# Optimization experiments

Hardware: AMD Instinct MI355X
Metric: run time of the kernel (lower is better)

## Reference

```python
import jax, jax.numpy as jnp
import numpy as np

HEADS = 20  # head_dim = 1280 // 20 = 64
LORA_SCALE = 1.0


def setup_inputs() -> dict:
    key = jax.random.key(0)
    ks = jax.random.split(key, 16)
    B, S, C, R = 2, 2048, 1280, 4
    w = 0.02  # keep activations numerically tame
    inp = {
        "x": jax.random.normal(ks[0], (B, S, C), jnp.float32),
        "Wq": jax.random.normal(ks[1], (C, C), jnp.float32) * w,
        "Wk": jax.random.normal(ks[2], (C, C), jnp.float32) * w,
        "Wv": jax.random.normal(ks[3], (C, C), jnp.float32) * w,
        "Wo": jax.random.normal(ks[4], (C, C), jnp.float32) * w,
        "bo": jnp.zeros((C,), jnp.float32),
        "Aq": jax.random.normal(ks[5], (R, C), jnp.float32) * w,
        "Bq": jax.random.normal(ks[6], (C, R), jnp.float32) * w,
        "Ak": jax.random.normal(ks[7], (R, C), jnp.float32) * w,
        "Bk": jax.random.normal(ks[8], (C, R), jnp.float32) * w,
        "Av": jax.random.normal(ks[9], (R, C), jnp.float32) * w,
        "Bv": jax.random.normal(ks[10], (C, R), jnp.float32) * w,
        "Ao": jax.random.normal(ks[11], (R, C), jnp.float32) * w,
        "Bo": jax.random.normal(ks[12], (C, R), jnp.float32) * w,
    }
    return inp


def _lora(x, A, B):
    # LoRALinearLayer: up(down(x)); network_alpha=None -> no extra scaling
    return (x @ A.T) @ B.T


def reference(x, Wq, Wk, Wv, Wo, bo, Aq, Bq, Ak, Bk, Av, Bv, Ao, Bo):
    B, S, C = x.shape
    H = HEADS
    D = C // H
    # base projections + LoRA updates (self-attention: encoder_hidden_states = x)
    q = x @ Wq.T + LORA_SCALE * _lora(x, Aq, Bq)
    k = x @ Wk.T + LORA_SCALE * _lora(x, Ak, Bk)
    v = x @ Wv.T + LORA_SCALE * _lora(x, Av, Bv)
    # head split: [B, S, H, D]
    q = q.reshape(B, S, H, D)
    k = k.reshape(B, S, H, D)
    v = v.reshape(B, S, H, D)
    # explicit scores + softmax (attn.get_attention_scores), scale = 1/sqrt(D)
    scale = 1.0 / jnp.sqrt(jnp.asarray(D, x.dtype))
    scores = jnp.einsum("bshd,bthd->bhst", q, k) * scale  # [B, H, S, S]
    probs = jax.nn.softmax(scores, axis=-1)
    ctx = jnp.einsum("bhst,bthd->bshd", probs, v).reshape(B, S, C)
    # output projection (+bias) + LoRA; dropout is identity at eval
    out = ctx @ Wo.T + bo + LORA_SCALE * _lora(ctx, Ao, Bo)
    return out
```

## Files before the change

### kernel.cpp

```cpp
#include <hip/hip_runtime.h>

#define BATCH 2
#define SEQ   2048
#define CH    1280
#define NH    20
#define HD    64
#define BS    (BATCH*SEQ)
#define RK    4

typedef __attribute__((ext_vector_type(2)))  float floatx2;
typedef __attribute__((ext_vector_type(4)))  short bf16x4;
typedef __attribute__((ext_vector_type(8)))  short bf16x8;
typedef __attribute__((ext_vector_type(16))) float floatx16;

__device__ __forceinline__ floatx16 mfma32(bf16x8 a, bf16x8 b, floatx16 c) {
    return __builtin_amdgcn_mfma_f32_32x32x16_bf16(a, b, c, 0, 0, 0);
}
__device__ __forceinline__ floatx16 mfma32k8(bf16x4 a, bf16x4 b, floatx16 c) {
    return __builtin_amdgcn_mfma_f32_32x32x8bf16_1k(a, b, c, 0, 0, 0);
}

__device__ __forceinline__ unsigned short f2bf(float f) {
    unsigned int u = __float_as_uint(f);
    u += 0x7fffu + ((u >> 16) & 1u);
    return (unsigned short)(u >> 16);
}
__device__ __forceinline__ unsigned int packbf(float hi, float lo) {
    unsigned int a = __float_as_uint(hi) + 0x8000u;
    unsigned int b = __float_as_uint(lo) + 0x8000u;
    return __builtin_amdgcn_perm(a, b, 0x07060302u);
}
__device__ __forceinline__ float fexp2(float x) {
#if __has_builtin(__builtin_amdgcn_exp2f)
    return __builtin_amdgcn_exp2f(x);
#else
    return exp2f(x);
#endif
}

__device__ __forceinline__ void cp16(const unsigned short* g, unsigned short* l) {
    __builtin_amdgcn_global_load_lds(
        (const __attribute__((address_space(1))) unsigned int*)g,
        (__attribute__((address_space(3))) unsigned int*)l, 16, 0, 0);
}

__global__ __launch_bounds__(256) void fold_weights(
    const float* __restrict__ Wq, const float* __restrict__ Wk,
    const float* __restrict__ Wv, const float* __restrict__ Wo,
    const float* __restrict__ Aq, const float* __restrict__ Bq,
    const float* __restrict__ Ak, const float* __restrict__ Bk,
    const float* __restrict__ Av, const float* __restrict__ Bv,
    const float* __restrict__ Ao, const float* __restrict__ Bo,
    unsigned short* __restrict__ wq_bf, unsigned short* __restrict__ wk_bf,
    unsigned short* __restrict__ wv_bf, unsigned short* __restrict__ wo_bf)
{
    int e = blockIdx.x * 256 + threadIdx.x;
    int which = blockIdx.y;
    int i = e / CH, j = e % CH;
    const float *W, *A, *Bm;
    unsigned short* o;
    if (which == 0)      { W = Wq; A = Aq; Bm = Bq; o = wq_bf; }
    else if (which == 1) { W = Wk; A = Ak; Bm = Bk; o = wk_bf; }
    else if (which == 2) { W = Wv; A = Av; Bm = Bv; o = wv_bf; }
    else                 { W = Wo; A = Ao; Bm = Bo; o = wo_bf; }
    float acc = W[e];
#pragma unroll
    for (int r = 0; r < RK; r++) acc += Bm[i * RK + r] * A[r * CH + j];
    o[e] = f2bf(acc);
}

__global__ __launch_bounds__(256) void cast_x(const float* __restrict__ x,
                                              unsigned short* __restrict__ xb)
{
    int idx = (blockIdx.x * 256 + threadIdx.x) * 4;
    float4 v = *(const float4*)(x + idx);
    ushort4 o;
    o.x = f2bf(v.x); o.y = f2bf(v.y); o.z = f2bf(v.z); o.w = f2bf(v.w);
    *(ushort4*)(xb + idx) = o;
}

template<bool OUTF>
__device__ __forceinline__ void gemm128(
    const unsigned short* __restrict__ A, const unsigned short* __restrict__ B,
    unsigned short* __restrict__ obf, float* __restrict__ of,
    const float* __restrict__ bias, float oscale)
{
    __shared__ __align__(16) unsigned short sa[128 * 64];
    __shared__ __align__(16) unsigned short sb[128 * 64];
    const int tid = threadIdx.x;
    const int wav = tid >> 6, lane = tid & 63;
    const int n32 = lane & 31, half = lane >> 5;
    const int wr = wav >> 1, wc = wav & 1;
    const int M0 = blockIdx.y * 128, N0 = blockIdx.x * 128;

    const unsigned short* ga[4]; const unsigned short* gb[4];
    unsigned short* la[4]; unsigned short* lb[4];
#pragma unroll
    for (int g = 0; g < 4; g++) {
        int s = g * 256 + tid;
        int row = s >> 3, cc = (s & 7) ^ (row & 7);
        ga[g] = A + (size_t)(M0 + row) * CH + cc * 8;
        gb[g] = B + (size_t)(N0 + row) * CH + cc * 8;
        la[g] = sa + (size_t)(g * 256 + wav * 64) * 8;
        lb[g] = sb + (size_t)(g * 256 + wav * 64) * 8;
    }

    const int arow0 = wr * 64 + n32, brow0 = wc * 64 + n32;

    floatx16 acc[2][2];
#pragma unroll
    for (int mt = 0; mt < 2; mt++)
#pragma unroll
        for (int nt = 0; nt < 2; nt++)
#pragma unroll
            for (int r = 0; r < 16; r++) acc[mt][nt][r] = 0.f;

    for (int k0 = 0; k0 < CH; k0 += 64) {
#pragma unroll
        for (int g = 0; g < 4; g++) { cp16(ga[g], la[g]); cp16(gb[g], lb[g]); }
#pragma unroll
        for (int g = 0; g < 4; g++) { ga[g] += 64; gb[g] += 64; }
        __syncthreads();

        bf16x8 av[2][4], bv[2][4];
#pragma unroll
        for (int mt = 0; mt < 2; mt++) {
            const int ar = arow0 + mt * 32, br = brow0 + mt * 32;
#pragma unroll
            for (int ks = 0; ks < 4; ks++) {
                const int cc = ks * 2 + half;
                av[mt][ks] = *(const bf16x8*)(sa + ar * 64 + ((cc ^ (ar & 7)) << 3));
                bv[mt][ks] = *(const bf16x8*)(sb + br * 64 + ((cc ^ (br & 7)) << 3));
            }
        }
#pragma unroll
        for (int ks = 0; ks < 4; ks++)
#pragma unroll
            for (int mt = 0; mt < 2; mt++)
#pragma unroll
                for (int nt = 0; nt < 2; nt++)
                    acc[mt][nt] = mfma32(av[mt][ks], bv[nt][ks], acc[mt][nt]);
        __syncthreads();
    }

#pragma unroll
    for (int mt = 0; mt < 2; mt++) {
#pragma unroll
        for (int nt = 0; nt < 2; nt++) {
            const int col = N0 + wc * 64 + nt * 32 + n32;
            const float bv2 = OUTF ? bias[col] : 0.f;
#pragma unroll
            for (int r = 0; r < 16; r++) {
                size_t row = (size_t)(M0 + wr * 64 + mt * 32 +
                                      (r & 3) + 8 * (r >> 2) + 4 * half);
                if (OUTF) of[row * CH + col] = acc[mt][nt][r] + bv2;
                else      obf[row * CH + col] = f2bf(acc[mt][nt][r] * oscale);
            }
        }
    }
}

__global__ __launch_bounds__(256) void gemm_qkv(
    const unsigned short* __restrict__ xb,
    const unsigned short* __restrict__ wq, const unsigned short* __restrict__ wk,
    const unsigned short* __restrict__ wv,
    unsigned short* __restrict__ q, unsigned short* __restrict__ k,
    unsigned short* __restrict__ v)
{
    const unsigned short* w = blockIdx.z == 0 ? wq : blockIdx.z == 1 ? wk : wv;
    unsigned short* o = blockIdx.z == 0 ? q : blockIdx.z == 1 ? k : v;
    float scale = blockIdx.z == 0 ? 0.18033688011112042f : 1.0f;
    gemm128<false>(xb, w, o, nullptr, nullptr, scale);
}

__global__ __launch_bounds__(256) void gemm_o(
    const unsigned short* __restrict__ c_bf, const unsigned short* __restrict__ wo,
    const float* __restrict__ bias, float* __restrict__ out)
{
    gemm128<true>(c_bf, wo, nullptr, out, bias, 1.0f);
}

__global__ __launch_bounds__(256) void transpose_v(
    const unsigned short* __restrict__ v, unsigned short* __restrict__ vt)
{
    __shared__ unsigned short lds[32][34];
    const int s0 = blockIdx.x * 32;
    const int d0 = blockIdx.y * 32;
    const int bh = blockIdx.z, b = bh / NH, h = bh % NH;
    const int c = threadIdx.x & 31;
    const int rbase = threadIdx.x >> 5;
#pragma unroll
    for (int i = 0; i < 4; i++) {
        int r = rbase + i * 8;
        lds[r][c] = v[(size_t)(b * SEQ + s0 + r) * CH + h * HD + d0 + c];
    }
    __syncthreads();
    const int cperm = (c & ~12) | ((c & 4) << 1) | ((c & 8) >> 1);
#pragma unroll
    for (int i = 0; i < 4; i++) {
        int r = rbase + i * 8;
        vt[(size_t)(bh * HD + d0 + r) * SEQ + s0 + cperm] = lds[c][r];
    }
}

__global__ __launch_bounds__(256) void attention(
    const unsigned short* __restrict__ q, const unsigned short* __restrict__ k,
    const unsigned short* __restrict__ vt, unsigned short* __restrict__ c_bf)
{
    __shared__ __align__(16) unsigned short k_lds[128 * 64];
    __shared__ __align__(16) unsigned short v_lds[64 * 128];

    const int tid = threadIdx.x, wav = tid >> 6, lane = tid & 63;
    const int n32 = lane & 31, half = lane >> 5;
    const int q0 = blockIdx.x * 128;
    const int bh = blockIdx.y, b = bh / NH, h = bh % NH;

    const size_t qrow = (size_t)(b * SEQ + q0 + wav * 32 + n32);
    bf16x8 qf[4];
#pragma unroll
    for (int f = 0; f < 4; f++)
        qf[f] = *(const bf16x8*)(q + qrow * CH + h * HD + f * 16 + half * 8);

    const unsigned short* gk[4]; const unsigned short* gv[4];
    unsigned short* lk[4]; unsigned short* lv[4];
#pragma unroll
    for (int g = 0; g < 4; g++) {
        int s = g * 256 + tid;
        int rowk = s >> 3, cck = (s & 7) ^ (rowk & 7);
        gk[g] = k + (size_t)(b * SEQ + rowk) * CH + h * HD + cck * 8;
        lk[g] = k_lds + (size_t)(g * 256 + wav * 64) * 8;
        int rowv = s >> 4, ccv = (s & 15) ^ (rowv & 15);
        gv[g] = vt + (size_t)(bh * HD + rowv) * SEQ + ccv * 8;
        lv[g] = v_lds + (size_t)(g * 256 + wav * 64) * 8;
    }

    floatx2 ps = {0.f, 0.f};
    floatx16 acc[2];
#pragma unroll
    for (int dt = 0; dt < 2; dt++)
#pragma unroll
        for (int r = 0; r < 16; r++) acc[dt][r] = 0.f;

    for (int t0 = 0; t0 < SEQ; t0 += 128) {
#pragma unroll
        for (int g = 0; g < 4; g++) { cp16(gk[g], lk[g]); cp16(gv[g], lv[g]); }
#pragma unroll
        for (int g = 0; g < 4; g++) { gk[g] += (size_t)128 * CH; gv[g] += 128; }
        __syncthreads();

#pragma unroll
        for (int kt = 0; kt < 4; kt++) {
            const int keyrow = kt * 32 + n32;
            const unsigned short* kr = k_lds + keyrow * 64;
            floatx16 st;
#pragma unroll
            for (int r = 0; r < 16; r++) st[r] = 0.f;
#pragma unroll
            for (int f = 0; f < 4; f++) {
                int phys = (2 * f + half) ^ (keyrow & 7);
                bf16x8 kf = *(const bf16x8*)(kr + phys * 8);
                st = mfma32(kf, qf[f], st);
            }

            float p[16];
#pragma unroll
            for (int r = 0; r < 16; r++) p[r] = fexp2(st[r]);
            unsigned int pk[8];
#pragma unroll
            for (int j = 0; j < 8; j++) {
                ps += (floatx2){p[2 * j], p[2 * j + 1]};
                pk[j] = packbf(p[2 * j + 1], p[2 * j]);
            }

#pragma unroll
            for (int dt = 0; dt < 2; dt++) {
                const int drow = dt * 32 + n32;
                const unsigned short* vr = v_lds + drow * 128;
#pragma unroll
                for (int pp = 0; pp < 2; pp++) {
                    int ct = kt * 4 + pp * 2 + half;
                    int phys = ct ^ (drow & 15);
                    union { bf16x8 v8; bf16x4 v4[2]; } vv;
                    vv.v8 = *(const bf16x8*)(vr + phys * 8);
                    union { unsigned int u[2]; bf16x4 v; } pb0, pb1;
                    pb0.u[0] = pk[4 * pp + 0]; pb0.u[1] = pk[4 * pp + 1];
                    pb1.u[0] = pk[4 * pp + 2]; pb1.u[1] = pk[4 * pp + 3];
                    acc[dt] = mfma32k8(vv.v4[0], pb0.v, acc[dt]);
                    acc[dt] = mfma32k8(vv.v4[1], pb1.v, acc[dt]);
                }
            }
        }
        __syncthreads();
    }

    float psum = ps.x + ps.y;
    float tot = psum + __shfl_xor(psum, 32, 64);
    float rinv = __frcp_rn(tot);
    const size_t obase = qrow * CH + h * HD;
#pragma unroll
    for (int dt = 0; dt < 2; dt++) {
#pragma unroll
        for (int jj = 0; jj < 4; jj++) {
            int d = dt * 32 + 8 * jj + 4 * half;
            uint2 o2;
            o2.x = packbf(acc[dt][4 * jj + 1] * rinv, acc[dt][4 * jj + 0] * rinv);
            o2.y = packbf(acc[dt][4 * jj + 3] * rinv, acc[dt][4 * jj + 2] * rinv);
            *(uint2*)(c_bf + obase + d) = o2;
        }
    }
}

extern "C" void kernel_launch(void* const* d_in, const int* in_sizes, int n_in,
                              void* d_out, int out_size, void* d_ws, size_t ws_size,
                              hipStream_t stream)
{
    const float* x  = (const float*)d_in[0];
    const float* Wq = (const float*)d_in[1];
    const float* Wk = (const float*)d_in[2];
    const float* Wv = (const float*)d_in[3];
    const float* Wo = (const float*)d_in[4];
    const float* bo = (const float*)d_in[5];
    const float* Aq = (const float*)d_in[6];
    const float* Bq = (const float*)d_in[7];
    const float* Ak = (const float*)d_in[8];
    const float* Bk = (const float*)d_in[9];
    const float* Av = (const float*)d_in[10];
    const float* Bv = (const float*)d_in[11];
    const float* Ao = (const float*)d_in[12];
    const float* Bo = (const float*)d_in[13];
    float* out = (float*)d_out;

    char* ws = (char*)d_ws;
    size_t off = 0;
    auto alloc = [&](size_t bytes) -> void* {
        void* p = ws + off; off += (bytes + 255) & ~(size_t)255; return p;
    };
    const size_t WB = (size_t)CH * CH, XB = (size_t)BS * CH;
    unsigned short* wq_bf = (unsigned short*)alloc(WB * 2);
    unsigned short* wk_bf = (unsigned short*)alloc(WB * 2);
    unsigned short* wv_bf = (unsigned short*)alloc(WB * 2);
    unsigned short* wo_bf = (unsigned short*)alloc(WB * 2);
    unsigned short* x_bf  = (unsigned short*)alloc(XB * 2);
    unsigned short* q_bf  = (unsigned short*)alloc(XB * 2);
    unsigned short* k_bf  = (unsigned short*)alloc(XB * 2);
    unsigned short* v_bf  = (unsigned short*)alloc(XB * 2);
    unsigned short* vt_bf = (unsigned short*)alloc(XB * 2);
    unsigned short* c_bf  = (unsigned short*)alloc(XB * 2);
    (void)ws_size; (void)n_in; (void)in_sizes; (void)out_size;

    fold_weights<<<dim3(CH * CH / 256, 4), 256, 0, stream>>>(
        Wq, Wk, Wv, Wo, Aq, Bq, Ak, Bk, Av, Bv, Ao, Bo,
        wq_bf, wk_bf, wv_bf, wo_bf);

    cast_x<<<dim3(BS * CH / 1024), 256, 0, stream>>>(x, x_bf);

    gemm_qkv<<<dim3(CH / 128, BS / 128, 3), 256, 0, stream>>>(
        x_bf, wq_bf, wk_bf, wv_bf, q_bf, k_bf, v_bf);

    transpose_v<<<dim3(SEQ / 32, 2, BATCH * NH), 256, 0, stream>>>(v_bf, vt_bf);

    attention<<<dim3(SEQ / 128, BATCH * NH), 256, 0, stream>>>(
        q_bf, k_bf, vt_bf, c_bf);

    gemm_o<<<dim3(CH / 128, BS / 128), 256, 0, stream>>>(c_bf, wo_bf, bo, out);
}
```

Before: 289.7 us.

## Merge prep kernels and cut attention register pressure for higher occupancy

Merges the weight-folding and x-cast kernels into one launch, which removes a kernel launch and its tail. In the attention kernel it replaces the per-group pointer arrays with a single base pointer plus constant offsets. It also computes exp and packing per half-tile right before use rather than materialising all 16 probabilities at once. It sets launch_bounds to 4 blocks per CU, so register usage is capped to raise occupancy, at some risk of spills.

```diff
diff --git a/kernel.cpp b/kernel.cpp
--- a/kernel.cpp
+++ b/kernel.cpp
@@ -44,7 +44,11 @@
         (__attribute__((address_space(3))) unsigned int*)l, 16, 0, 0);
 }
 
-__global__ __launch_bounds__(256) void fold_weights(
+#define FOLD_BLOCKS (CH * CH / 256)
+#define CAST_BLOCKS (BS * CH / 1024)
+
+__global__ __launch_bounds__(256) void prep(
+    const float* __restrict__ x,
     const float* __restrict__ Wq, const float* __restrict__ Wk,
     const float* __restrict__ Wv, const float* __restrict__ Wo,
     const float* __restrict__ Aq, const float* __restrict__ Bq,
@@ -52,31 +56,31 @@
     const float* __restrict__ Av, const float* __restrict__ Bv,
     const float* __restrict__ Ao, const float* __restrict__ Bo,
     unsigned short* __restrict__ wq_bf, unsigned short* __restrict__ wk_bf,
-    unsigned short* __restrict__ wv_bf, unsigned short* __restrict__ wo_bf)
-{
-    int e = blockIdx.x * 256 + threadIdx.x;
-    int which = blockIdx.y;
-    int i = e / CH, j = e % CH;
-    const float *W, *A, *Bm;
-    unsigned short* o;
-    if (which == 0)      { W = Wq; A = Aq; Bm = Bq; o = wq_bf; }
-    else if (which == 1) { W = Wk; A = Ak; Bm = Bk; o = wk_bf; }
-    else if (which == 2) { W = Wv; A = Av; Bm = Bv; o = wv_bf; }
-    else                 { W = Wo; A = Ao; Bm = Bo; o = wo_bf; }
-    float acc = W[e];
-#pragma unroll
-    for (int r = 0; r < RK; r++) acc += Bm[i * RK + r] * A[r * CH + j];
-    o[e] = f2bf(acc);
-}
-
-__global__ __launch_bounds__(256) void cast_x(const float* __restrict__ x,
-                                              unsigned short* __restrict__ xb)
-{
-    int idx = (blockIdx.x * 256 + threadIdx.x) * 4;
-    float4 v = *(const float4*)(x + idx);
-    ushort4 o;
-    o.x = f2bf(v.x); o.y = f2bf(v.y); o.z = f2bf(v.z); o.w = f2bf(v.w);
-    *(ushort4*)(xb + idx) = o;
+    unsigned short* __restrict__ wv_bf, unsigned short* __restrict__ wo_bf,
+    unsigned short* __restrict__ xb)
+{
+    const int bx = blockIdx.x;
+    if (bx < 4 * FOLD_BLOCKS) {
+        int which = bx / FOLD_BLOCKS;
+        int e = (bx % FOLD_BLOCKS) * 256 + threadIdx.x;
+        int i = e / CH, j = e % CH;
+        const float *W, *A, *Bm;
+        unsigned short* o;
+        if (which == 0)      { W = Wq; A = Aq; Bm = Bq; o = wq_bf; }
+        else if (which == 1) { W = Wk; A = Ak; Bm = Bk; o = wk_bf; }
+        else if (which == 2) { W = Wv; A = Av; Bm = Bv; o = wv_bf; }
+        else                 { W = Wo; A = Ao; Bm = Bo; o = wo_bf; }
+        float acc = W[e];
+#pragma unroll
+        for (int r = 0; r < RK; r++) acc += Bm[i * RK + r] * A[r * CH + j];
+        o[e] = f2bf(acc);
+    } else {
+        int idx = ((bx - 4 * FOLD_BLOCKS) * 256 + threadIdx.x) * 4;
+        float4 v = *(const float4*)(x + idx);
+        ushort4 o;
+        o.x = f2bf(v.x); o.y = f2bf(v.y); o.z = f2bf(v.z); o.w = f2bf(v.w);
+        *(ushort4*)(xb + idx) = o;
+    }
 }
 
 template<bool OUTF>
@@ -203,7 +207,7 @@
     }
 }
 
-__global__ __launch_bounds__(256) void attention(
+__global__ __launch_bounds__(256, 4) void attention(
     const unsigned short* __restrict__ q, const unsigned short* __restrict__ k,
     const unsigned short* __restrict__ vt, unsigned short* __restrict__ c_bf)
 {
@@ -221,18 +225,12 @@
     for (int f = 0; f < 4; f++)
         qf[f] = *(const bf16x8*)(q + qrow * CH + h * HD + f * 16 + half * 8);
 
-    const unsigned short* gk[4]; const unsigned short* gv[4];
-    unsigned short* lk[4]; unsigned short* lv[4];
-#pragma unroll
-    for (int g = 0; g < 4; g++) {
-        int s = g * 256 + tid;
-        int rowk = s >> 3, cck = (s & 7) ^ (rowk & 7);
-        gk[g] = k + (size_t)(b * SEQ + rowk) * CH + h * HD + cck * 8;
-        lk[g] = k_lds + (size_t)(g * 256 + wav * 64) * 8;
-        int rowv = s >> 4, ccv = (s & 15) ^ (rowv & 15);
-        gv[g] = vt + (size_t)(bh * HD + rowv) * SEQ + ccv * 8;
-        lv[g] = v_lds + (size_t)(g * 256 + wav * 64) * 8;
-    }
+    const int rowk = tid >> 3, cck = (tid & 7) ^ (rowk & 7);
+    const int rowv = tid >> 4, ccv = (tid & 15) ^ (rowv & 15);
+    const unsigned short* gk0 = k + (size_t)(b * SEQ + rowk) * CH + h * HD + cck * 8;
+    const unsigned short* gv0 = vt + (size_t)(bh * HD + rowv) * SEQ + ccv * 8;
+    unsigned short* lk0 = k_lds + (size_t)(wav * 64) * 8;
+    unsigned short* lv0 = v_lds + (size_t)(wav * 64) * 8;
 
     floatx2 ps = {0.f, 0.f};
     floatx16 acc[2];
@@ -243,9 +241,11 @@
 
     for (int t0 = 0; t0 < SEQ; t0 += 128) {
 #pragma unroll
-        for (int g = 0; g < 4; g++) { cp16(gk[g], lk[g]); cp16(gv[g], lv[g]); }
-#pragma unroll
-        for (int g = 0; g < 4; g++) { gk[g] += (size_t)128 * CH; gv[g] += 128; }
+        for (int g = 0; g < 4; g++) {
+            cp16(gk0 + (size_t)g * 32 * CH, lk0 + g * 2048);
+            cp16(gv0 + g * 16 * SEQ, lv0 + g * 2048);
+        }
+        gk0 += (size_t)128 * CH; gv0 += 128;
         __syncthreads();
 
 #pragma unroll
@@ -262,29 +262,27 @@
                 st = mfma32(kf, qf[f], st);
             }
 
-            float p[16];
-#pragma unroll
-            for (int r = 0; r < 16; r++) p[r] = fexp2(st[r]);
-            unsigned int pk[8];
-#pragma unroll
-            for (int j = 0; j < 8; j++) {
-                ps += (floatx2){p[2 * j], p[2 * j + 1]};
-                pk[j] = packbf(p[2 * j + 1], p[2 * j]);
-            }
-
-#pragma unroll
-            for (int dt = 0; dt < 2; dt++) {
-                const int drow = dt * 32 + n32;
-                const unsigned short* vr = v_lds + drow * 128;
-#pragma unroll
-                for (int pp = 0; pp < 2; pp++) {
+#pragma unroll
+            for (int pp = 0; pp < 2; pp++) {
+                float p[8];
+#pragma unroll
+                for (int r = 0; r < 8; r++) p[r] = fexp2(st[8 * pp + r]);
+                unsigned int pk[4];
+#pragma unroll
+                for (int j = 0; j < 4; j++) {
+                    ps += (floatx2){p[2 * j], p[2 * j + 1]};
+                    pk[j] = packbf(p[2 * j + 1], p[2 * j]);
+                }
+                union { unsigned int u[2]; bf16x4 v; } pb0, pb1;
+                pb0.u[0] = pk[0]; pb0.u[1] = pk[1];
+                pb1.u[0] = pk[2]; pb1.u[1] = pk[3];
+#pragma unroll
+                for (int dt = 0; dt < 2; dt++) {
+                    const int drow = dt * 32 + n32;
                     int ct = kt * 4 + pp * 2 + half;
                     int phys = ct ^ (drow & 15);
                     union { bf16x8 v8; bf16x4 v4[2]; } vv;
-                    vv.v8 = *(const bf16x8*)(vr + phys * 8);
-                    union { unsigned int u[2]; bf16x4 v; } pb0, pb1;
-                    pb0.u[0] = pk[4 * pp + 0]; pb0.u[1] = pk[4 * pp + 1];
-                    pb1.u[0] = pk[4 * pp + 2]; pb1.u[1] = pk[4 * pp + 3];
+                    vv.v8 = *(const bf16x8*)(v_lds + drow * 128 + phys * 8);
                     acc[dt] = mfma32k8(vv.v4[0], pb0.v, acc[dt]);
                     acc[dt] = mfma32k8(vv.v4[1], pb1.v, acc[dt]);
                 }
@@ -348,11 +346,9 @@
     unsigned short* c_bf  = (unsigned short*)alloc(XB * 2);
     (void)ws_size; (void)n_in; (void)in_sizes; (void)out_size;
 
-    fold_weights<<<dim3(CH * CH / 256, 4), 256, 0, stream>>>(
-        Wq, Wk, Wv, Wo, Aq, Bq, Ak, Bk, Av, Bv, Ao, Bo,
-        wq_bf, wk_bf, wv_bf, wo_bf);
-
-    cast_x<<<dim3(BS * CH / 1024), 256, 0, stream>>>(x, x_bf);
+    prep<<<dim3(4 * FOLD_BLOCKS + CAST_BLOCKS), 256, 0, stream>>>(
+        x, Wq, Wk, Wv, Wo, Aq, Bq, Ak, Bk, Av, Bv, Ao, Bo,
+        wq_bf, wk_bf, wv_bf, wo_bf, x_bf);
 
     gemm_qkv<<<dim3(CH / 128, BS / 128, 3), 256, 0, stream>>>(
         x_bf, wq_bf, wk_bf, wv_bf, q_bf, k_bf, v_bf);
```

Result: faster. 271.7 us (-6.2%).
